# Optimization experiments

Hardware: AMD Instinct MI355X
Metric: run time of the kernel (lower is better)

## Reference

```python
import jax, jax.numpy as jnp
import numpy as np

N = 50000        # nodes
E = 800000       # edges (avg degree 16)
F_IN = 128       # in_features
F_OUT = 64       # out_features per head
HEADS = 4        # SparseGATConv default n_heads
ALPHA = 0.01     # LeakyReLU negative slope (SparseGATConv default alpha)


def setup_inputs() -> dict:
    key = jax.random.key(0)
    ks = jax.random.split(key, 6)
    x = jax.random.normal(ks[0], (N, F_IN), dtype=jnp.float32)
    edge_index = jax.random.randint(ks[1], (2, E), 0, N, dtype=jnp.int64)
    # xavier-normal-ish init, gain 1.414 as in the torch module
    W_heads = jax.random.normal(ks[2], (HEADS, F_IN, F_OUT), dtype=jnp.float32) * (1.414 / np.sqrt(F_IN))
    attn_heads = jax.random.normal(ks[3], (HEADS, 2 * F_OUT, 1), dtype=jnp.float32) * 0.1
    W_out = jax.random.normal(ks[4], (HEADS * F_OUT, F_OUT), dtype=jnp.float32) * (1.414 / np.sqrt(HEADS * F_OUT))
    attn_out = jax.random.normal(ks[5], (2 * F_OUT, 1), dtype=jnp.float32) * 0.1
    return {"x": x, "edge_index": edge_index, "W_heads": W_heads,
            "attn_heads": attn_heads, "W_out": W_out, "attn_out": attn_out}


def _sp_gat_layer(x, src, dst, W, attn, concat):
    """SpGraphAttentionLayer.forward: dense x @ W, edge attention scores,
    sparse row-softmax over COO adjacency, sparse-mm aggregation."""
    h = x @ W                                   # (N, d)
    d = h.shape[1]
    # cat(h[src], h[dst]) @ attn  ==  (h@a1)[src] + (h@a2)[dst]  (avoids (E,2d) concat)
    s1 = (h @ attn[:d]).squeeze(-1)             # (N,)
    s2 = (h @ attn[d:]).squeeze(-1)             # (N,)
    scores = -jax.nn.leaky_relu(s1[src] + s2[dst], negative_slope=ALPHA)  # (E,)
    # torch.sparse.softmax(dim=1): softmax over existing entries in each row (src)
    row_max = jax.ops.segment_max(scores, src, num_segments=N)
    ex = jnp.exp(scores - row_max[src])
    denom = jax.ops.segment_sum(ex, src, num_segments=N)
    a = ex / denom[src]                         # (E,) edge attention weights
    # sparse.mm: out[i] = sum_{e: src[e]=i} a[e] * h[dst[e]]
    out = jax.ops.segment_sum(a[:, None] * h[dst], src, num_segments=N)  # (N, d)
    return jax.nn.elu(out) if concat else out


def reference(x, edge_index, W_heads, attn_heads, W_out, attn_out):
    src, dst = edge_index[0], edge_index[1]
    # multi-head GAT layers (concat=True), then out_att on concatenated features
    heads_out = jax.vmap(lambda W, a: _sp_gat_layer(x, src, dst, W, a, True))(W_heads, attn_heads)  # (H, N, F_OUT)
    hcat = jnp.transpose(heads_out, (1, 0, 2)).reshape(N, HEADS * F_OUT)  # matches torch.cat(dim=1) head order
    return _sp_gat_layer(hcat, src, dst, W_out, attn_out, False)          # (N, F_OUT)
```

## Files before the change

kernel.cpp:

```cpp
#include <hip/hip_runtime.h>

typedef unsigned short u16;
typedef _Float16 f16;
typedef __attribute__((ext_vector_type(8))) _Float16 f16x8;
typedef __attribute__((ext_vector_type(2))) _Float16 f16x2;
typedef __attribute__((ext_vector_type(4))) float f32x4;

__device__ inline float nlrelu(float z) { return (z > 0.f) ? -z : -0.01f * z; }
__device__ inline float4 score4(float4 a, float4 b) {
    return make_float4(nlrelu(a.x + b.x), nlrelu(a.y + b.y), nlrelu(a.z + b.z), nlrelu(a.w + b.w));
}
__device__ inline unsigned packdup(float w) {
    f16x2 p = (f16x2){(f16)w, (f16)w};
    return __builtin_bit_cast(unsigned, p);
}

__global__ void k_init(const float* __restrict__ Wh, const float* __restrict__ Wo,
                       f16* __restrict__ B1, f16* __restrict__ B2,
                       int* __restrict__ counts, int N) {
    const int b = blockIdx.x;
    if (b < 128) {
        int i = b * 256 + threadIdx.x;
        int j = i & 7, lane = (i >> 3) & 63, kg = (i >> 9) & 3, nt = i >> 11;
        int n = nt * 16 + (lane & 15);
        int k = kg * 32 + ((lane >> 4) << 3) + j;
        B1[i] = (f16)Wh[(n >> 6) * (128 * 64) + k * 64 + (n & 63)];
    } else if (b < 192) {
        int i = (b - 128) * 256 + threadIdx.x;
        int j = i & 7, lane = (i >> 3) & 63, kg = (i >> 9) & 7, nt = i >> 12;
        int n = nt * 16 + (lane & 15);
        int k = kg * 32 + ((lane >> 4) << 3) + j;
        B2[i] = (f16)Wo[k * 64 + n];
    } else {
        int i = (b - 192) * 256 + threadIdx.x;
        if (i < N) counts[i] = 0;
    }
}

__global__ __launch_bounds__(256) void count_pos(const int* __restrict__ src, int* __restrict__ counts,
                                                 int* __restrict__ pos, int E, int N) {
    const int base = blockIdx.x * 1024 + threadIdx.x;
#pragma unroll
    for (int j = 0; j < 4; j++) {
        int e = base + j * 256;
        if (e < E) {
            int s = src[e];
            s = ((unsigned)s < (unsigned)N) ? s : 0;
            pos[e] = atomicAdd(&counts[s], 1);
        }
    }
}

__global__ __launch_bounds__(1024) void scan_p1(const int* __restrict__ counts, int* __restrict__ rowst,
                                                int* __restrict__ bsum, int n) {
    const int t = threadIdx.x, lane = t & 63, w = t >> 6;
    __shared__ int wsum[16];
    int i = blockIdx.x * 1024 + t;
    int v = (i < n) ? counts[i] : 0;
    int orig = v;
    for (int d = 1; d < 64; d <<= 1) { int x = __shfl_up(v, d); if (lane >= d) v += x; }
    if (lane == 63) wsum[w] = v;
    __syncthreads();
    if (t == 0) {
        int acc = 0;
        for (int j = 0; j < 16; j++) { int tmp = wsum[j]; wsum[j] = acc; acc += tmp; }
        bsum[blockIdx.x] = acc;
    }
    __syncthreads();
    if (i < n) rowst[i] = wsum[w] + (v - orig);
}

__global__ void scan_p3(const int* __restrict__ bsum, int* __restrict__ rowst, int n, int nb) {
    __shared__ int sh_pre, sh_tot;
    const int i = blockIdx.x * 256 + threadIdx.x;
    const int g = (blockIdx.x * 256) >> 10;
    if (threadIdx.x == 0) {
        int acc = 0, pre = 0;
        for (int j = 0; j < nb; j++) { if (j == g) pre = acc; acc += bsum[j]; }
        if (g >= nb) pre = acc;
        sh_pre = pre; sh_tot = acc;
    }
    __syncthreads();
    if (i < n) rowst[i] += sh_pre;
    else if (i == n) rowst[n] = sh_tot;
}

__global__ __launch_bounds__(256) void scatter_noat(const int* __restrict__ src, const int* __restrict__ dst,
                                                    const int* __restrict__ rowst, const int* __restrict__ pos,
                                                    int* __restrict__ edged, int E, int N) {
    const int base = blockIdx.x * 1024 + threadIdx.x;
#pragma unroll
    for (int j = 0; j < 4; j++) {
        int e = base + j * 256;
        if (e < E) {
            int s = src[e];
            s = ((unsigned)s < (unsigned)N) ? s : 0;
            int d = dst[e];
            d = ((unsigned)d < (unsigned)N) ? d : 0;
            edged[rowst[s] + pos[e]] = d;
        }
    }
}

__global__ __launch_bounds__(256) void gemm1_f16(const float* __restrict__ X, const f16* __restrict__ B1,
        const float* __restrict__ attnH,
        f16* __restrict__ H1, float* __restrict__ s1, float* __restrict__ s2, int M) {
    const int lane = threadIdx.x & 63, wave = threadIdx.x >> 6;
    const int row0 = (blockIdx.x * 4 + wave) * 16;
    if (row0 >= M) return;
    const int mrow = row0 + (lane & 15);
    const int koff = (lane >> 4) * 8;
    const float* aptr = X + (size_t)mrow * 128 + koff;

    f32x4 acc[16];
#pragma unroll
    for (int c = 0; c < 16; c++) acc[c] = (f32x4){0.f, 0.f, 0.f, 0.f};

#pragma unroll
    for (int kg = 0; kg < 4; kg++) {
        float av[8];
        *(float4*)av       = *(const float4*)(aptr + kg * 32);
        *(float4*)(av + 4) = *(const float4*)(aptr + kg * 32 + 4);
        f16x8 a;
#pragma unroll
        for (int j = 0; j < 8; j++) a[j] = (f16)av[j];
#pragma unroll
        for (int nt = 0; nt < 16; nt++) {
            const size_t bidx = (size_t)(((nt << 2) + kg) * 64 + lane) * 8;
            f16x8 bfr = *(const f16x8*)(B1 + bidx);
            acc[nt] = __builtin_amdgcn_mfma_f32_16x16x32_f16(a, bfr, acc[nt], 0, 0, 0);
        }
    }
    const int rbase = (lane >> 4) * 4;
    const int colq = lane & 15;
#pragma unroll
    for (int h = 0; h < 4; h++) {
        float s1a[4] = {0.f, 0.f, 0.f, 0.f}, s2a[4] = {0.f, 0.f, 0.f, 0.f};
#pragma unroll
        for (int q = 0; q < 4; q++) {
            const int nt = h * 4 + q;
            const int col = nt * 16 + colq;
            const float a1v = attnH[h * 128 + (col & 63)];
            const float a2v = attnH[h * 128 + 64 + (col & 63)];
#pragma unroll
            for (int r = 0; r < 4; r++) {
                float c = acc[nt][r];
                H1[(size_t)(row0 + rbase + r) * 256 + col] = (f16)c;
                s1a[r] += c * a1v;
                s2a[r] += c * a2v;
            }
        }
#pragma unroll
        for (int off = 1; off < 16; off <<= 1)
#pragma unroll
            for (int r = 0; r < 4; r++) {
                s1a[r] += __shfl_xor(s1a[r], off);
                s2a[r] += __shfl_xor(s2a[r], off);
            }
        if (colq == 0)
#pragma unroll
            for (int r = 0; r < 4; r++) {
                s1[(size_t)(row0 + rbase + r) * 4 + h] = s1a[r];
                s2[(size_t)(row0 + rbase + r) * 4 + h] = s2a[r];
            }
    }
}

__global__ __launch_bounds__(256) void gemm2_f16(const f16* __restrict__ Hc, const f16* __restrict__ B2,
        const float* __restrict__ attnO,
        f16* __restrict__ H2, float* __restrict__ s1b, float* __restrict__ s2b, int M) {
    const int lane = threadIdx.x & 63, wave = threadIdx.x >> 6;
    const int row0 = (blockIdx.x * 4 + wave) * 16;
    if (row0 >= M) return;
    const int mrow = row0 + (lane & 15);
    const int koff = (lane >> 4) * 8;
    const f16* ap = Hc + (size_t)mrow * 256 + koff;

    f32x4 acc[4];
#pragma unroll
    for (int c = 0; c < 4; c++) acc[c] = (f32x4){0.f, 0.f, 0.f, 0.f};

#pragma unroll
    for (int kg = 0; kg < 8; kg++) {
        f16x8 a = *(const f16x8*)(ap + kg * 32);
#pragma unroll
        for (int nt = 0; nt < 4; nt++) {
            const size_t bidx = (size_t)(((nt << 3) + kg) * 64 + lane) * 8;
            f16x8 bfr = *(const f16x8*)(B2 + bidx);
            acc[nt] = __builtin_amdgcn_mfma_f32_16x16x32_f16(a, bfr, acc[nt], 0, 0, 0);
        }
    }
    const int rbase = (lane >> 4) * 4;
    const int colq = lane & 15;
    float s1a[4] = {0.f, 0.f, 0.f, 0.f}, s2a[4] = {0.f, 0.f, 0.f, 0.f};
#pragma unroll
    for (int nt = 0; nt < 4; nt++) {
        const int col = nt * 16 + colq;
        const float a1v = attnO[col];
        const float a2v = attnO[64 + col];
#pragma unroll
        for (int r = 0; r < 4; r++) {
            float c = acc[nt][r];
            H2[(size_t)(row0 + rbase + r) * 64 + col] = (f16)c;
            s1a[r] += c * a1v;
            s2a[r] += c * a2v;
        }
    }
#pragma unroll
    for (int off = 1; off < 16; off <<= 1)
#pragma unroll
        for (int r = 0; r < 4; r++) {
            s1a[r] += __shfl_xor(s1a[r], off);
            s2a[r] += __shfl_xor(s2a[r], off);
        }
    if (colq == 0)
#pragma unroll
        for (int r = 0; r < 4; r++) {
            s1b[row0 + rbase + r] = s1a[r];
            s2b[row0 + rbase + r] = s2a[r];
        }
}

__global__ __launch_bounds__(256) void agg_l1(const int* __restrict__ rowst, const int* __restrict__ edged,
                                              const float* __restrict__ s1, const float* __restrict__ s2,
                                              const f16* __restrict__ H, f16* __restrict__ hcat, int N) {
    __shared__ unsigned wls[4][64][4];
    __shared__ int dls[4][64];
    const int t = threadIdx.x, lane = t & 63, wave = t >> 6;
    const int node = blockIdx.x * 4 + wave;
    if (node >= N) return;
    const int beg = rowst[node], end = rowst[node + 1];
    const int deg = end - beg;
    const int head = lane >> 4;
    f16* outp = hcat + (size_t)node * 256 + lane * 4;
    if (deg == 0) { *(uint2*)outp = make_uint2(0u, 0u); return; }
    const float4 s1v = *(const float4*)(s1 + (size_t)node * 4);

    float r0, r1, r2, r3;
    if (deg <= 64) {
        int d = 0;
        if (lane < deg) d = edged[beg + lane];
        dls[wave][lane] = d;
        float4 s2v = *(const float4*)(s2 + (size_t)d * 4);
        float4 sc = score4(s1v, s2v);
        if (lane >= deg) sc = make_float4(-3e38f, -3e38f, -3e38f, -3e38f);
        float4 m = sc;
#pragma unroll
        for (int off = 32; off > 0; off >>= 1) {
            m.x = fmaxf(m.x, __shfl_xor(m.x, off));
            m.y = fmaxf(m.y, __shfl_xor(m.y, off));
            m.z = fmaxf(m.z, __shfl_xor(m.z, off));
            m.w = fmaxf(m.w, __shfl_xor(m.w, off));
        }
        float4 ex = make_float4(0.f, 0.f, 0.f, 0.f);
        if (lane < deg) ex = make_float4(__expf(sc.x - m.x), __expf(sc.y - m.y),
                                         __expf(sc.z - m.z), __expf(sc.w - m.w));
        float4 sm = ex;
#pragma unroll
        for (int off = 32; off > 0; off >>= 1) {
            sm.x += __shfl_xor(sm.x, off);
            sm.y += __shfl_xor(sm.y, off);
            sm.z += __shfl_xor(sm.z, off);
            sm.w += __shfl_xor(sm.w, off);
        }
        wls[wave][lane][0] = packdup(ex.x / sm.x);
        wls[wave][lane][1] = packdup(ex.y / sm.y);
        wls[wave][lane][2] = packdup(ex.z / sm.z);
        wls[wave][lane][3] = packdup(ex.w / sm.w);
        f16x2 a01[4], a23[4];
#pragma unroll
        for (int j = 0; j < 4; j++) { a01[j] = (f16x2)(f16)0.f; a23[j] = (f16x2)(f16)0.f; }
        int e = 0;
        for (; e + 4 <= deg; e += 4) {
#pragma unroll
            for (int j = 0; j < 4; j++) {
                int dd = dls[wave][e + j];
                uint2 raw = *(const uint2*)(H + (size_t)dd * 256 + lane * 4);
                f16x2 lo = __builtin_bit_cast(f16x2, raw.x);
                f16x2 hi = __builtin_bit_cast(f16x2, raw.y);
                f16x2 w2 = __builtin_bit_cast(f16x2, wls[wave][e + j][head]);
                a01[j] += w2 * lo;
                a23[j] += w2 * hi;
            }
        }
        for (; e < deg; e++) {
            int dd = dls[wave][e];
            uint2 raw = *(const uint2*)(H + (size_t)dd * 256 + lane * 4);
            f16x2 lo = __builtin_bit_cast(f16x2, raw.x);
            f16x2 hi = __builtin_bit_cast(f16x2, raw.y);
            f16x2 w2 = __builtin_bit_cast(f16x2, wls[wave][e][head]);
            a01[0] += w2 * lo;
            a23[0] += w2 * hi;
        }
        r0 = (float)a01[0][0] + (float)a01[1][0] + (float)a01[2][0] + (float)a01[3][0];
        r1 = (float)a01[0][1] + (float)a01[1][1] + (float)a01[2][1] + (float)a01[3][1];
        r2 = (float)a23[0][0] + (float)a23[1][0] + (float)a23[2][0] + (float)a23[3][0];
        r3 = (float)a23[0][1] + (float)a23[1][1] + (float)a23[2][1] + (float)a23[3][1];
    } else {
        float4 m = make_float4(-3e38f, -3e38f, -3e38f, -3e38f);
        for (int e = beg + lane; e < end; e += 64) {
            int d = edged[e];
            float4 sc = score4(s1v, *(const float4*)(s2 + (size_t)d * 4));
            m.x = fmaxf(m.x, sc.x); m.y = fmaxf(m.y, sc.y); m.z = fmaxf(m.z, sc.z); m.w = fmaxf(m.w, sc.w);
        }
#pragma unroll
        for (int off = 32; off > 0; off >>= 1) {
            m.x = fmaxf(m.x, __shfl_xor(m.x, off));
            m.y = fmaxf(m.y, __shfl_xor(m.y, off));
            m.z = fmaxf(m.z, __shfl_xor(m.z, off));
            m.w = fmaxf(m.w, __shfl_xor(m.w, off));
        }
        float4 sm = make_float4(0.f, 0.f, 0.f, 0.f);
        for (int e = beg + lane; e < end; e += 64) {
            int d = edged[e];
            float4 sc = score4(s1v, *(const float4*)(s2 + (size_t)d * 4));
            sm.x += __expf(sc.x - m.x); sm.y += __expf(sc.y - m.y);
            sm.z += __expf(sc.z - m.z); sm.w += __expf(sc.w - m.w);
        }
#pragma unroll
        for (int off = 32; off > 0; off >>= 1) {
            sm.x += __shfl_xor(sm.x, off);
            sm.y += __shfl_xor(sm.y, off);
            sm.z += __shfl_xor(sm.z, off);
            sm.w += __shfl_xor(sm.w, off);
        }
        float4 inv = make_float4(1.f / sm.x, 1.f / sm.y, 1.f / sm.z, 1.f / sm.w);
        float4 acc = make_float4(0.f, 0.f, 0.f, 0.f);
        for (int e = beg; e < end; e++) {
            int dd = edged[e];
            float4 sc = score4(s1v, *(const float4*)(s2 + (size_t)dd * 4));
            float wv[4] = { __expf(sc.x - m.x) * inv.x, __expf(sc.y - m.y) * inv.y,
                            __expf(sc.z - m.z) * inv.z, __expf(sc.w - m.w) * inv.w };
            float w = (head == 0) ? wv[0] : (head == 1) ? wv[1] : (head == 2) ? wv[2] : wv[3];
            const f16* hp = H + (size_t)dd * 256 + lane * 4;
            acc.x += w * (float)hp[0]; acc.y += w * (float)hp[1];
            acc.z += w * (float)hp[2]; acc.w += w * (float)hp[3];
        }
        r0 = acc.x; r1 = acc.y; r2 = acc.z; r3 = acc.w;
    }
    r0 = (r0 > 0.f) ? r0 : (__expf(r0) - 1.f);
    r1 = (r1 > 0.f) ? r1 : (__expf(r1) - 1.f);
    r2 = (r2 > 0.f) ? r2 : (__expf(r2) - 1.f);
    r3 = (r3 > 0.f) ? r3 : (__expf(r3) - 1.f);
    f16x2 o0 = (f16x2){(f16)r0, (f16)r1};
    f16x2 o1 = (f16x2){(f16)r2, (f16)r3};
    *(uint2*)outp = make_uint2(__builtin_bit_cast(unsigned, o0), __builtin_bit_cast(unsigned, o1));
}

__global__ __launch_bounds__(256) void agg_l2(const int* __restrict__ rowst, const int* __restrict__ edged,
                                              const float* __restrict__ s1, const float* __restrict__ s2,
                                              const f16* __restrict__ H, float* __restrict__ outp, int N) {
    __shared__ float wls[4][64];
    __shared__ int dls[4][64];
    const int t = threadIdx.x, lane = t & 63, wave = t >> 6;
    const int node = blockIdx.x * 4 + wave;
    if (node >= N) return;
    const int beg = rowst[node], end = rowst[node + 1];
    const int deg = end - beg;
    if (deg == 0) { outp[(size_t)node * 64 + lane] = 0.f; return; }
    const float s1v = s1[node];

    float acc = 0.f;
    if (deg <= 64) {
        int d = 0;
        if (lane < deg) d = edged[beg + lane];
        dls[wave][lane] = d;
        float z = s1v + s2[d];
        float sc = (lane < deg) ? nlrelu(z) : -3e38f;
        float m = sc;
#pragma unroll
        for (int off = 32; off > 0; off >>= 1) m = fmaxf(m, __shfl_xor(m, off));
        float ex = (lane < deg) ? __expf(sc - m) : 0.f;
        float sm = ex;
#pragma unroll
        for (int off = 32; off > 0; off >>= 1) sm += __shfl_xor(sm, off);
        wls[wave][lane] = ex / sm;
        int e = 0;
        for (; e + 4 <= deg; e += 4) {
            int d0 = dls[wave][e], d1 = dls[wave][e + 1], d2 = dls[wave][e + 2], d3 = dls[wave][e + 3];
            float h0 = (float)H[(size_t)d0 * 64 + lane];
            float h1 = (float)H[(size_t)d1 * 64 + lane];
            float h2 = (float)H[(size_t)d2 * 64 + lane];
            float h3 = (float)H[(size_t)d3 * 64 + lane];
            acc += wls[wave][e] * h0 + wls[wave][e + 1] * h1 + wls[wave][e + 2] * h2 + wls[wave][e + 3] * h3;
        }
        for (; e < deg; e++)
            acc += wls[wave][e] * (float)H[(size_t)dls[wave][e] * 64 + lane];
    } else {
        float m = -3e38f;
        for (int e = beg + lane; e < end; e += 64) {
            int d = edged[e];
            m = fmaxf(m, nlrelu(s1v + s2[d]));
        }
#pragma unroll
        for (int off = 32; off > 0; off >>= 1) m = fmaxf(m, __shfl_xor(m, off));
        float sm = 0.f;
        for (int e = beg + lane; e < end; e += 64) {
            int d = edged[e];
            sm += __expf(nlrelu(s1v + s2[d]) - m);
        }
#pragma unroll
        for (int off = 32; off > 0; off >>= 1) sm += __shfl_xor(sm, off);
        float inv = 1.f / sm;
        for (int e = beg; e < end; e++) {
            int dd = edged[e];
            float w = __expf(nlrelu(s1v + s2[dd]) - m) * inv;
            acc += w * (float)H[(size_t)dd * 64 + lane];
        }
    }
    outp[(size_t)node * 64 + lane] = acc;
}

extern "C" void kernel_launch(void* const* d_in, const int* in_sizes, int n_in,
                              void* d_out, int out_size, void* d_ws, size_t ws_size,
                              hipStream_t stream) {
    const float* x     = (const float*)d_in[0];
    const int*   ei    = (const int*)d_in[1];
    const float* Wh    = (const float*)d_in[2];
    const float* attnH = (const float*)d_in[3];
    const float* Wo    = (const float*)d_in[4];
    const float* attnO = (const float*)d_in[5];
    float* out         = (float*)d_out;

    const int N = in_sizes[0] / 128;
    const int E = in_sizes[1] / 2;
    const int* srcp = ei;
    const int* dstp = ei + E;

    char* base = (char*)d_ws;
    size_t off = 0;
    auto take = [&](size_t b) { void* p = base + off; off += (b + 255) & ~(size_t)255; return p; };
    f16*   B1     = (f16*)  take(32768 * 2);
    f16*   B2     = (f16*)  take(16384 * 2);
    int*   counts = (int*)  take((size_t)N * 4);
    int*   rowst  = (int*)  take((size_t)(N + 1) * 4);
    int*   pos    = (int*)  take((size_t)E * 4);
    int*   edged  = (int*)  take((size_t)E * 4);
    int*   bsum   = (int*)  take(4096);
    float* s1     = (float*)take((size_t)N * 4 * 4);
    float* s2     = (float*)take((size_t)N * 4 * 4);
    float* s1b    = (float*)take((size_t)N * 4);
    float* s2b    = (float*)take((size_t)N * 4);
    f16*   H1     = (f16*)  take((size_t)N * 256 * 2);
    f16*   hcat   = (f16*)  take((size_t)N * 256 * 2);
    f16*   H2     = (f16*)  take((size_t)N * 64 * 2);

    const int zb = (N + 255) / 256;
    k_init<<<192 + zb, 256, 0, stream>>>(Wh, Wo, B1, B2, counts, N);

    const int eb4 = (E + 1023) / 1024;
    count_pos<<<eb4, 256, 0, stream>>>(srcp, counts, pos, E, N);

    const int nb = (N + 1023) / 1024;
    scan_p1<<<nb, 1024, 0, stream>>>(counts, rowst, bsum, N);
    scan_p3<<<(N + 256) / 256, 256, 0, stream>>>(bsum, rowst, N, nb);

    scatter_noat<<<eb4, 256, 0, stream>>>(srcp, dstp, rowst, pos, edged, E, N);

    const int Gg = (N + 63) / 64;
    gemm1_f16<<<Gg, 256, 0, stream>>>(x, B1, attnH, H1, s1, s2, N);
    agg_l1<<<(N + 3) / 4, 256, 0, stream>>>(rowst, edged, s1, s2, H1, hcat, N);
    gemm2_f16<<<Gg, 256, 0, stream>>>(hcat, B2, attnO, H2, s1b, s2b, N);
    agg_l2<<<(N + 3) / 4, 256, 0, stream>>>(rowst, edged, s1b, s2b, H2, out, N);
}
```

Before: 262.9 us.

## Fuse count into init, replace two-pass scan with atomic ticket, batch gathers

Zeroes counts with memset and folds the atomic degree counting into the weight-conversion kernel. The two-pass prefix scan becomes a single pass in which each block claims its base offset with an atomicAdd on a cursor. Rows therefore sit in non-monotonic order, so the aggregation kernels read each node's degree from counts instead of rowst[node+1]. It also adds an 8-wide batched gather loop in agg_l1 to keep more loads in flight. The aim is fewer kernel launches and more memory parallelism, at the cost of CSR row order becoming nondeterministic.

```diff
diff --git a/kernel.cpp b/kernel.cpp
--- a/kernel.cpp
+++ b/kernel.cpp
@@ -15,9 +15,10 @@
     return __builtin_bit_cast(unsigned, p);
 }
 
-__global__ void k_init(const float* __restrict__ Wh, const float* __restrict__ Wo,
+__global__ __launch_bounds__(256) void k_initcnt(const float* __restrict__ Wh, const float* __restrict__ Wo,
                        f16* __restrict__ B1, f16* __restrict__ B2,
-                       int* __restrict__ counts, int N) {
+                       const int* __restrict__ src, int* __restrict__ counts, int* __restrict__ pos,
+                       int E, int N) {
     const int b = blockIdx.x;
     if (b < 128) {
         int i = b * 256 + threadIdx.x;
@@ -32,29 +33,24 @@
         int k = kg * 32 + ((lane >> 4) << 3) + j;
         B2[i] = (f16)Wo[k * 64 + n];
     } else {
-        int i = (b - 192) * 256 + threadIdx.x;
-        if (i < N) counts[i] = 0;
-    }
-}
-
-__global__ __launch_bounds__(256) void count_pos(const int* __restrict__ src, int* __restrict__ counts,
-                                                 int* __restrict__ pos, int E, int N) {
-    const int base = blockIdx.x * 1024 + threadIdx.x;
-#pragma unroll
-    for (int j = 0; j < 4; j++) {
-        int e = base + j * 256;
-        if (e < E) {
-            int s = src[e];
-            s = ((unsigned)s < (unsigned)N) ? s : 0;
-            pos[e] = atomicAdd(&counts[s], 1);
-        }
-    }
-}
-
-__global__ __launch_bounds__(1024) void scan_p1(const int* __restrict__ counts, int* __restrict__ rowst,
-                                                int* __restrict__ bsum, int n) {
+        const int base = (b - 192) * 1024 + threadIdx.x;
+#pragma unroll
+        for (int j = 0; j < 4; j++) {
+            int e = base + j * 256;
+            if (e < E) {
+                int s = src[e];
+                s = ((unsigned)s < (unsigned)N) ? s : 0;
+                pos[e] = atomicAdd(&counts[s], 1);
+            }
+        }
+    }
+}
+
+__global__ __launch_bounds__(1024) void scan_ticket(const int* __restrict__ counts, int* __restrict__ rowst,
+                                                    int* __restrict__ cursor, int n) {
     const int t = threadIdx.x, lane = t & 63, w = t >> 6;
     __shared__ int wsum[16];
+    __shared__ int sh_base;
     int i = blockIdx.x * 1024 + t;
     int v = (i < n) ? counts[i] : 0;
     int orig = v;
@@ -64,25 +60,10 @@
     if (t == 0) {
         int acc = 0;
         for (int j = 0; j < 16; j++) { int tmp = wsum[j]; wsum[j] = acc; acc += tmp; }
-        bsum[blockIdx.x] = acc;
+        sh_base = atomicAdd(cursor, acc);
     }
     __syncthreads();
-    if (i < n) rowst[i] = wsum[w] + (v - orig);
-}
-
-__global__ void scan_p3(const int* __restrict__ bsum, int* __restrict__ rowst, int n, int nb) {
-    __shared__ int sh_pre, sh_tot;
-    const int i = blockIdx.x * 256 + threadIdx.x;
-    const int g = (blockIdx.x * 256) >> 10;
-    if (threadIdx.x == 0) {
-        int acc = 0, pre = 0;
-        for (int j = 0; j < nb; j++) { if (j == g) pre = acc; acc += bsum[j]; }
-        if (g >= nb) pre = acc;
-        sh_pre = pre; sh_tot = acc;
-    }
-    __syncthreads();
-    if (i < n) rowst[i] += sh_pre;
-    else if (i == n) rowst[n] = sh_tot;
+    if (i < n) rowst[i] = sh_base + wsum[w] + (v - orig);
 }
 
 __global__ __launch_bounds__(256) void scatter_noat(const int* __restrict__ src, const int* __restrict__ dst,
@@ -221,7 +202,8 @@
         }
 }
 
-__global__ __launch_bounds__(256) void agg_l1(const int* __restrict__ rowst, const int* __restrict__ edged,
+__global__ __launch_bounds__(256) void agg_l1(const int* __restrict__ rowst, const int* __restrict__ cnt,
+                                              const int* __restrict__ edged,
                                               const float* __restrict__ s1, const float* __restrict__ s2,
                                               const f16* __restrict__ H, f16* __restrict__ hcat, int N) {
     __shared__ unsigned wls[4][64][4];
@@ -229,8 +211,9 @@
     const int t = threadIdx.x, lane = t & 63, wave = t >> 6;
     const int node = blockIdx.x * 4 + wave;
     if (node >= N) return;
-    const int beg = rowst[node], end = rowst[node + 1];
-    const int deg = end - beg;
+    const int beg = rowst[node];
+    const int deg = cnt[node];
+    const int end = beg + deg;
     const int head = lane >> 4;
     f16* outp = hcat + (size_t)node * 256 + lane * 4;
     if (deg == 0) { *(uint2*)outp = make_uint2(0u, 0u); return; }
@@ -271,6 +254,20 @@
 #pragma unroll
         for (int j = 0; j < 4; j++) { a01[j] = (f16x2)(f16)0.f; a23[j] = (f16x2)(f16)0.f; }
         int e = 0;
+        for (; e + 8 <= deg; e += 8) {
+            uint2 raw[8];
+#pragma unroll
+            for (int j = 0; j < 8; j++)
+                raw[j] = *(const uint2*)(H + (size_t)dls[wave][e + j] * 256 + lane * 4);
+#pragma unroll
+            for (int j = 0; j < 8; j++) {
+                f16x2 lo = __builtin_bit_cast(f16x2, raw[j].x);
+                f16x2 hi = __builtin_bit_cast(f16x2, raw[j].y);
+                f16x2 w2 = __builtin_bit_cast(f16x2, wls[wave][e + j][head]);
+                a01[j & 3] += w2 * lo;
+                a23[j & 3] += w2 * hi;
+            }
+        }
         for (; e + 4 <= deg; e += 4) {
 #pragma unroll
             for (int j = 0; j < 4; j++) {
@@ -347,7 +344,8 @@
     *(uint2*)outp = make_uint2(__builtin_bit_cast(unsigned, o0), __builtin_bit_cast(unsigned, o1));
 }
 
-__global__ __launch_bounds__(256) void agg_l2(const int* __restrict__ rowst, const int* __restrict__ edged,
+__global__ __launch_bounds__(256) void agg_l2(const int* __restrict__ rowst, const int* __restrict__ cnt,
+                                              const int* __restrict__ edged,
                                               const float* __restrict__ s1, const float* __restrict__ s2,
                                               const f16* __restrict__ H, float* __restrict__ outp, int N) {
     __shared__ float wls[4][64];
@@ -355,8 +353,9 @@
     const int t = threadIdx.x, lane = t & 63, wave = t >> 6;
     const int node = blockIdx.x * 4 + wave;
     if (node >= N) return;
-    const int beg = rowst[node], end = rowst[node + 1];
-    const int deg = end - beg;
+    const int beg = rowst[node];
+    const int deg = cnt[node];
+    const int end = beg + deg;
     if (deg == 0) { outp[(size_t)node * 64 + lane] = 0.f; return; }
     const float s1v = s1[node];
 
@@ -433,10 +432,10 @@
     f16*   B1     = (f16*)  take(32768 * 2);
     f16*   B2     = (f16*)  take(16384 * 2);
     int*   counts = (int*)  take((size_t)N * 4);
-    int*   rowst  = (int*)  take((size_t)(N + 1) * 4);
+    int*   rowst  = (int*)  take((size_t)N * 4);
     int*   pos    = (int*)  take((size_t)E * 4);
     int*   edged  = (int*)  take((size_t)E * 4);
-    int*   bsum   = (int*)  take(4096);
+    int*   cursor = (int*)  take(256);
     float* s1     = (float*)take((size_t)N * 4 * 4);
     float* s2     = (float*)take((size_t)N * 4 * 4);
     float* s1b    = (float*)take((size_t)N * 4);
@@ -445,21 +444,20 @@
     f16*   hcat   = (f16*)  take((size_t)N * 256 * 2);
     f16*   H2     = (f16*)  take((size_t)N * 64 * 2);
 
-    const int zb = (N + 255) / 256;
-    k_init<<<192 + zb, 256, 0, stream>>>(Wh, Wo, B1, B2, counts, N);
+    hipMemsetAsync(counts, 0, (size_t)N * 4, stream);
+    hipMemsetAsync(cursor, 0, 4, stream);
 
     const int eb4 = (E + 1023) / 1024;
-    count_pos<<<eb4, 256, 0, stream>>>(srcp, counts, pos, E, N);
+    k_initcnt<<<192 + eb4, 256, 0, stream>>>(Wh, Wo, B1, B2, srcp, counts, pos, E, N);
 
     const int nb = (N + 1023) / 1024;
-    scan_p1<<<nb, 1024, 0, stream>>>(counts, rowst, bsum, N);
-    scan_p3<<<(N + 256) / 256, 256, 0, stream>>>(bsum, rowst, N, nb);
+    scan_ticket<<<nb, 1024, 0, stream>>>(counts, rowst, cursor, N);
 
     scatter_noat<<<eb4, 256, 0, stream>>>(srcp, dstp, rowst, pos, edged, E, N);
 
     const int Gg = (N + 63) / 64;
     gemm1_f16<<<Gg, 256, 0, stream>>>(x, B1, attnH, H1, s1, s2, N);
-    agg_l1<<<(N + 3) / 4, 256, 0, stream>>>(rowst, edged, s1, s2, H1, hcat, N);
+    agg_l1<<<(N + 3) / 4, 256, 0, stream>>>(rowst, counts, edged, s1, s2, H1, hcat, N);
     gemm2_f16<<<Gg, 256, 0, stream>>>(hcat, B2, attnO, H2, s1b, s2b, N);
-    agg_l2<<<(N + 3) / 4, 256, 0, stream>>>(rowst, edged, s1b, s2b, H2, out, N);
-}
+    agg_l2<<<(N + 3) / 4, 256, 0, stream>>>(rowst, counts, edged, s1b, s2b, H2, out, N);
+}
```

Result: faster. 257.2 us (-2.2%).
